# Optimization experiments

Hardware: AMD Instinct MI355X
Metric: run time of the kernel (lower is better)

The kernel has to match this reference:

```python
import jax, jax.numpy as jnp
import numpy as np

B, C, H, W = 16, 64, 256, 256
M1, M2 = 32, 32
SCALE = 1.0 / (C * C)


def setup_inputs() -> dict:
    key = jax.random.key(0)
    ks = jax.random.split(key, 5)
    x = jax.random.normal(ks[0], (B, C, H, W), dtype=jnp.float32)
    w1_real = SCALE * jax.random.uniform(ks[1], (C, C, M1, M2), dtype=jnp.float32)
    w1_imag = SCALE * jax.random.uniform(ks[2], (C, C, M1, M2), dtype=jnp.float32)
    w2_real = SCALE * jax.random.uniform(ks[3], (C, C, M1, M2), dtype=jnp.float32)
    w2_imag = SCALE * jax.random.uniform(ks[4], (C, C, M1, M2), dtype=jnp.float32)
    return {"x": x, "w1_real": w1_real, "w1_imag": w1_imag,
            "w2_real": w2_real, "w2_imag": w2_imag}


def reference(x, w1_real, w1_imag, w2_real, w2_imag):
    # x: (B, C, H, W) real. rfft2 over last two dims -> (B, C, H, W//2+1) complex64
    x_ft = jnp.fft.rfft2(x)
    # compl_mul2d in the source reduces to an elementwise multiply by the
    # weights summed over their FIRST (in_channels) axis:
    #   out[b,c,m1,m2] = x_ft[b,c,m1,m2] * sum_j weights[j,c,m1,m2]
    w1 = (w1_real + 1j * w1_imag).sum(axis=0)  # (C, M1, M2) complex
    w2 = (w2_real + 1j * w2_imag).sum(axis=0)  # (C, M1, M2) complex
    out_ft = jnp.zeros_like(x_ft)
    out_ft = out_ft.at[:, :, :M1, :M2].set(x_ft[:, :, :M1, :M2] * w1[None])
    out_ft = out_ft.at[:, :, -M1:, :M2].set(x_ft[:, :, -M1:, :M2] * w2[None])
    return jnp.fft.irfft2(out_ft, s=(H, W))
```

## Files before the change

kernel.cpp:

```cpp
#include <hip/hip_runtime.h>
#include <math.h>

#define TWO_PI 6.28318530717958647692f

typedef __attribute__((ext_vector_type(8))) short bf16x8;
typedef __attribute__((ext_vector_type(4))) float f32x4;
typedef __attribute__((ext_vector_type(4))) short short4v;

#define MFMA16(A,B,C) __builtin_amdgcn_mfma_f32_16x16x32_bf16((A),(B),(C),0,0,0)


#define C_B2H 0
#define C_B2L 16384
#define C_C1H 32768
#define C_C1L 49152
#define C_S1H 65536
#define C_S1L 81920
#define C_SNH 98304
#define C_SNL 114688
#define C_A1H 131072
#define C_A1L 163840
#define C_DH  196608
#define C_DL  212992

__device__ __forceinline__ unsigned short bhi(float v) {
    union { float f; unsigned u; } x; x.f = v;
    return (unsigned short)(x.u >> 16);
}
__device__ __forceinline__ float bval(unsigned short h) {
    union { unsigned u; float f; } x; x.u = ((unsigned)h) << 16;
    return x.f;
}
__device__ __forceinline__ void split2(float v, unsigned short& hi, unsigned short& lo) {
    hi = bhi(v);
    lo = bhi(v - bval(hi));
}

__global__ __launch_bounds__(256)
void const_kernel(unsigned short* __restrict__ cst) {
    int e = blockIdx.x * 256 + threadIdx.x;
    const float w0 = TWO_PI / 256.0f;
    float v; int i, baseH, baseL;
    if (e < 16384) {
        i = e; baseH = C_B2H; baseL = C_B2L;
        int j = i & 7, lane = (i >> 3) & 63, tt = i >> 9;
        int nt = tt & 3, kt = tt >> 2;
        int k = kt * 32 + (lane >> 4) * 8 + j;
        int n = nt * 16 + (lane & 15);
        int fr = n & 31;
        float s_, c_;
        sincosf(w0 * (float)((fr * k) & 255), &s_, &c_);
        v = (n < 32) ? c_ : -s_;
    } else if (e < 65536) {
        int mid = (e - 16384) >> 14;
        i = (e - 16384) & 16383;
        baseH = C_C1H + mid * 32768; baseL = baseH + 16384;
        int j = i & 7, lane = (i >> 3) & 63, tt = i >> 9;
        int mt = tt & 3, kt = tt >> 2;
        int s = mt * 16 + (lane & 15);
        int h = kt * 32 + (lane >> 4) * 8 + j;
        int f = (s < 32) ? s : s + 192;
        float s_, c_;
        sincosf(w0 * (float)((f * h) & 255), &s_, &c_);
        v = (mid == 0) ? c_ : ((mid == 1) ? s_ : -s_);
    } else if (e < 98304) {
        i = e - 65536; baseH = C_A1H; baseL = C_A1L;
        int j = i & 7, lane = (i >> 3) & 63, tt = i >> 9;
        int mt = tt & 15, kt = tt >> 4;
        int h = mt * 16 + (lane & 15);
        int k = kt * 32 + (lane >> 4) * 8 + j;
        int s = k & 63;
        int f = (s < 32) ? s : s + 192;
        float s_, c_;
        sincosf(w0 * (float)((f * h) & 255), &s_, &c_);
        v = (k < 64) ? c_ : s_;
    } else {
        i = e - 98304; baseH = C_DH; baseL = C_DL;
        int j = i & 7, lane = (i >> 3) & 63, tt = i >> 9;
        int nt = tt & 15, kt = tt >> 4;
        int wc = nt * 16 + (lane & 15);
        int k = kt * 32 + (lane >> 4) * 8 + j;
        int k2 = k & 31;
        float a = (k2 == 0) ? 1.f : 2.f;
        float s_, c_;
        sincosf(w0 * (float)((k2 * wc) & 255), &s_, &c_);
        v = (k < 32) ? a * c_ : -a * s_;
    }
    unsigned short hi, lo; split2(v, hi, lo);
    cst[baseH + i] = hi;
    cst[baseL + i] = lo;
}

__global__ __launch_bounds__(256)
void wsum_part(const float* __restrict__ w1r, const float* __restrict__ w1i,
               const float* __restrict__ w2r, const float* __restrict__ w2i,
               float4* __restrict__ part) {
    const int jp = blockIdx.x >> 6;
    const int e4 = (blockIdx.x & 63) * 256 + threadIdx.x;
    const float4* A = (const float4*)w1r;
    const float4* Bv = (const float4*)w1i;
    const float4* Cv = (const float4*)w2r;
    const float4* Dv = (const float4*)w2i;
    float4 a = make_float4(0.f,0.f,0.f,0.f), b = a, c = a, d = a;
    #pragma unroll
    for (int jj = 0; jj < 8; ++jj) {
        int idx = (jp * 8 + jj) * 16384 + e4;
        float4 v;
        v = A[idx];  a.x += v.x; a.y += v.y; a.z += v.z; a.w += v.w;
        v = Bv[idx]; b.x += v.x; b.y += v.y; b.z += v.z; b.w += v.w;
        v = Cv[idx]; c.x += v.x; c.y += v.y; c.z += v.z; c.w += v.w;
        v = Dv[idx]; d.x += v.x; d.y += v.y; d.z += v.z; d.w += v.w;
    }
    part[(0 * 8 + jp) * 16384 + e4] = a;
    part[(1 * 8 + jp) * 16384 + e4] = b;
    part[(2 * 8 + jp) * 16384 + e4] = c;
    part[(3 * 8 + jp) * 16384 + e4] = d;
}

__global__ __launch_bounds__(256)
void wsum_reduce(const float4* __restrict__ part,
                 float4* __restrict__ s1, float4* __restrict__ s2) {
    const int e4 = blockIdx.x * 256 + threadIdx.x;
    float4 a = make_float4(0.f,0.f,0.f,0.f), b = a, c = a, d = a;
    #pragma unroll
    for (int jp = 0; jp < 8; ++jp) {
        float4 v;
        v = part[(0 * 8 + jp) * 16384 + e4]; a.x += v.x; a.y += v.y; a.z += v.z; a.w += v.w;
        v = part[(1 * 8 + jp) * 16384 + e4]; b.x += v.x; b.y += v.y; b.z += v.z; b.w += v.w;
        v = part[(2 * 8 + jp) * 16384 + e4]; c.x += v.x; c.y += v.y; c.z += v.z; c.w += v.w;
        v = part[(3 * 8 + jp) * 16384 + e4]; d.x += v.x; d.y += v.y; d.z += v.z; d.w += v.w;
    }
    const float sc = 1.0f / 65536.0f;
    s1[e4 * 2]     = make_float4(a.x * sc, b.x * sc, a.y * sc, b.y * sc);
    s1[e4 * 2 + 1] = make_float4(a.z * sc, b.z * sc, a.w * sc, b.w * sc);
    s2[e4 * 2]     = make_float4(c.x * sc, d.x * sc, c.y * sc, d.y * sc);
    s2[e4 * 2 + 1] = make_float4(c.z * sc, d.z * sc, c.w * sc, d.w * sc);
}

__global__ __launch_bounds__(256)
void fwd_kernel(const float* __restrict__ x, float* __restrict__ X,
                const unsigned short* __restrict__ cst) {
    const int img = blockIdx.x;
    const int t = threadIdx.x;
    const int lane = t & 63;
    const int wv = t >> 6;

    __shared__ unsigned short xs_hi[8192], xs_lo[8192];
    __shared__ unsigned short yt_hi[2048], yt_lo[2048];

    f32x4 acc[4];
    #pragma unroll
    for (int i = 0; i < 4; ++i) { acc[i].x = 0; acc[i].y = 0; acc[i].z = 0; acc[i].w = 0; }

    const int mt2  = wv >> 1;
    const int nt2b = (wv & 1) * 2;

    const float* xim = x + (size_t)img * 65536;
    const int r_st  = t >> 3;
    const int c4_st = t & 7;
    const float4* src = (const float4*)xim + r_st * 64 + c4_st;

    float4 pre[8];
    #pragma unroll
    for (int i = 0; i < 8; ++i) pre[i] = src[i * 8];

    #pragma unroll 1
    for (int hc = 0; hc < 8; ++hc) {
        {
            #pragma unroll
            for (int i = 0; i < 8; ++i) {
                float4 vx = pre[i];
                int cc = (c4_st + i * 8) * 4;
                int idx = (r_st * 256 + cc) ^ ((r_st & 7) << 3);
                unsigned short h0,l0,h1,l1,h2,l2,h3,l3;
                split2(vx.x, h0, l0); split2(vx.y, h1, l1);
                split2(vx.z, h2, l2); split2(vx.w, h3, l3);
                short4v vh, vl;
                vh.x=(short)h0; vh.y=(short)h1; vh.z=(short)h2; vh.w=(short)h3;
                vl.x=(short)l0; vl.y=(short)l1; vl.z=(short)l2; vl.w=(short)l3;
                *(short4v*)&xs_hi[idx] = vh;
                *(short4v*)&xs_lo[idx] = vl;
            }
        }
        __syncthreads();
        if (hc < 7) {
            const float4* nsrc = src + (hc + 1) * 2048;
            #pragma unroll
            for (int i = 0; i < 8; ++i) pre[i] = nsrc[i * 8];
        }
        f32x4 acc2[2];
        acc2[0].x=0; acc2[0].y=0; acc2[0].z=0; acc2[0].w=0;
        acc2[1].x=0; acc2[1].y=0; acc2[1].z=0; acc2[1].w=0;
        {
            const int mrow = mt2 * 16 + (lane & 15);
            const int kb = (lane >> 4) * 8;
            #pragma unroll
            for (int kt = 0; kt < 8; ++kt) {
                int aidx = (mrow * 256 + kt * 32 + kb) ^ ((mrow & 7) << 3);
                bf16x8 ah = *(const bf16x8*)&xs_hi[aidx];
                bf16x8 al = *(const bf16x8*)&xs_lo[aidx];
                #pragma unroll
                for (int q = 0; q < 2; ++q) {
                    int boff = ((kt * 4 + nt2b + q) * 64 + lane) * 8;
                    bf16x8 bh = *(const bf16x8*)&cst[C_B2H + boff];
                    bf16x8 bl = *(const bf16x8*)&cst[C_B2L + boff];
                    acc2[q] = MFMA16(ah, bh, acc2[q]);
                    acc2[q] = MFMA16(ah, bl, acc2[q]);
                    acc2[q] = MFMA16(al, bh, acc2[q]);
                }
            }
        }
        {
            const int hbase = mt2 * 16 + (lane >> 4) * 4;
            #pragma unroll
            for (int q = 0; q < 2; ++q) {
                int n = (nt2b + q) * 16 + (lane & 15);
                int idx = (n * 32 + hbase) ^ ((n & 7) << 3);
                short4v vh, vl; unsigned short hh, ll;
                split2(acc2[q][0], hh, ll); vh.x=(short)hh; vl.x=(short)ll;
                split2(acc2[q][1], hh, ll); vh.y=(short)hh; vl.y=(short)ll;
                split2(acc2[q][2], hh, ll); vh.z=(short)hh; vl.z=(short)ll;
                split2(acc2[q][3], hh, ll); vh.w=(short)hh; vl.w=(short)ll;
                *(short4v*)&yt_hi[idx] = vh;
                *(short4v*)&yt_lo[idx] = vl;
            }
        }
        __syncthreads();
        {
            const int aoff = ((hc * 4 + wv) * 64 + lane) * 8;
            bf16x8 c1h = *(const bf16x8*)&cst[C_C1H + aoff];
            bf16x8 c1l = *(const bf16x8*)&cst[C_C1L + aoff];
            bf16x8 s1h = *(const bf16x8*)&cst[C_S1H + aoff];
            bf16x8 s1l = *(const bf16x8*)&cst[C_S1L + aoff];
            bf16x8 snh = *(const bf16x8*)&cst[C_SNH + aoff];
            bf16x8 snl = *(const bf16x8*)&cst[C_SNL + aoff];
            const int kl = (lane >> 4) * 8;
            #pragma unroll
            for (int nt = 0; nt < 4; ++nt) {
                int nRe = (nt & 1) * 16 + (lane & 15);
                int nIm = 32 + nRe;
                int reIdx = (nRe * 32 + kl) ^ ((nRe & 7) << 3);
                int imIdx = (nIm * 32 + kl) ^ ((nIm & 7) << 3);
                bf16x8 brh = *(const bf16x8*)&yt_hi[reIdx];
                bf16x8 brl = *(const bf16x8*)&yt_lo[reIdx];
                bf16x8 bih = *(const bf16x8*)&yt_hi[imIdx];
                bf16x8 bil = *(const bf16x8*)&yt_lo[imIdx];
                if (nt < 2) {
                    acc[nt] = MFMA16(c1h, brh, acc[nt]);
                    acc[nt] = MFMA16(c1h, brl, acc[nt]);
                    acc[nt] = MFMA16(c1l, brh, acc[nt]);
                    acc[nt] = MFMA16(s1h, bih, acc[nt]);
                    acc[nt] = MFMA16(s1h, bil, acc[nt]);
                    acc[nt] = MFMA16(s1l, bih, acc[nt]);
                } else {
                    acc[nt] = MFMA16(c1h, bih, acc[nt]);
                    acc[nt] = MFMA16(c1h, bil, acc[nt]);
                    acc[nt] = MFMA16(c1l, bih, acc[nt]);
                    acc[nt] = MFMA16(snh, brh, acc[nt]);
                    acc[nt] = MFMA16(snh, brl, acc[nt]);
                    acc[nt] = MFMA16(snl, brh, acc[nt]);
                }
            }
        }
        __syncthreads();
    }
    {
        float* Xp = X + (size_t)img * 4096;
        const int sbase = wv * 16 + (lane >> 4) * 4;
        #pragma unroll
        for (int nt = 0; nt < 4; ++nt) {
            int n = nt * 16 + (lane & 15);
            #pragma unroll
            for (int r = 0; r < 4; ++r)
                Xp[(sbase + r) * 64 + n] = acc[nt][r];
        }
    }
}

__global__ __launch_bounds__(256)
void inv_kernel(const float* __restrict__ X, const float2* __restrict__ s1,
                const float2* __restrict__ s2, float* __restrict__ out,
                const unsigned short* __restrict__ cst) {
    const int img = blockIdx.x;
    const int c = img & 63;
    const int t = threadIdx.x;
    const int lane = t & 63;
    const int wv = t >> 6;

    __shared__ unsigned short lds[32768];
    unsigned short* GTh = lds;
    unsigned short* GTl = lds + 8192;
    unsigned short* Th  = lds;
    unsigned short* Tl  = lds + 16384;

    {
        const float* Xp = X + (size_t)img * 4096;
        int s = t >> 2;
        int k2b = (t & 3) * 8;
        const float2* wp = (s < 32) ? (s1 + c * 1024 + s * 32 + k2b)
                                    : (s2 + c * 1024 + (s - 32) * 32 + k2b);
        float4 xr0 = *(const float4*)&Xp[s * 64 + k2b];
        float4 xr1 = *(const float4*)&Xp[s * 64 + k2b + 4];
        float4 xi0 = *(const float4*)&Xp[s * 64 + 32 + k2b];
        float4 xi1 = *(const float4*)&Xp[s * 64 + 32 + k2b + 4];
        float xr[8] = {xr0.x,xr0.y,xr0.z,xr0.w,xr1.x,xr1.y,xr1.z,xr1.w};
        float xi[8] = {xi0.x,xi0.y,xi0.z,xi0.w,xi1.x,xi1.y,xi1.z,xi1.w};
        #pragma unroll
        for (int i = 0; i < 8; ++i) {
            int k2 = k2b + i;
            float2 wvv = wp[i];
            float gr = xr[i]*wvv.x - xi[i]*wvv.y;
            float gi = xr[i]*wvv.y + xi[i]*wvv.x;
            unsigned short grh, grl, gih, gil;
            split2(gr, grh, grl); split2(gi, gih, gil);
            int swz = (k2 & 7) << 3;
            int i0 = (k2 * 128 + s) ^ swz;
            int i1 = ((32 + k2) * 128 + s) ^ swz;
            int i2 = (k2 * 128 + 64 + s) ^ swz;
            int i3 = ((32 + k2) * 128 + 64 + s) ^ swz;
            GTh[i0] = grh; GTl[i0] = grl;
            GTh[i1] = gih; GTl[i1] = gil;
            GTh[i2] = (unsigned short)(gih ^ 0x8000u);
            GTl[i2] = (unsigned short)(gil ^ 0x8000u);
            GTh[i3] = grh; GTl[i3] = grl;
        }
    }
    __syncthreads();

    f32x4 Tacc[4][4];
    #pragma unroll
    for (int a = 0; a < 4; ++a)
        #pragma unroll
        for (int b = 0; b < 4; ++b) { Tacc[a][b].x=0; Tacc[a][b].y=0; Tacc[a][b].z=0; Tacc[a][b].w=0; }
    {
        const int kb = (lane >> 4) * 8;
        #pragma unroll
        for (int kt = 0; kt < 4; ++kt) {
            bf16x8 bh[4], bl[4];
            #pragma unroll
            for (int nt = 0; nt < 4; ++nt) {
                int n = nt * 16 + (lane & 15);
                int idx = (n * 128 + kt * 32 + kb) ^ ((n & 7) << 3);
                bh[nt] = *(const bf16x8*)&GTh[idx];
                bl[nt] = *(const bf16x8*)&GTl[idx];
            }
            #pragma unroll
            for (int mi = 0; mi < 4; ++mi) {
                int aoff = ((kt * 16 + 4 * wv + mi) * 64 + lane) * 8;
                bf16x8 ah = *(const bf16x8*)&cst[C_A1H + aoff];
                bf16x8 al = *(const bf16x8*)&cst[C_A1L + aoff];
                #pragma unroll
                for (int nt = 0; nt < 4; ++nt) {
                    Tacc[mi][nt] = MFMA16(ah, bh[nt], Tacc[mi][nt]);
                    Tacc[mi][nt] = MFMA16(ah, bl[nt], Tacc[mi][nt]);
                    Tacc[mi][nt] = MFMA16(al, bh[nt], Tacc[mi][nt]);
                }
            }
        }
    }
    __syncthreads();

    {
        #pragma unroll
        for (int mi = 0; mi < 4; ++mi) {
            int m0 = (4 * wv + mi) * 16 + (lane >> 4) * 4;
            #pragma unroll
            for (int nt = 0; nt < 4; ++nt) {
                int k = nt * 16 + (lane & 15);
                #pragma unroll
                for (int r = 0; r < 4; ++r) {
                    int m = m0 + r;
                    int idx = (m * 64 + k) ^ ((m & 7) << 3);
                    unsigned short hh, ll; split2(Tacc[mi][nt][r], hh, ll);
                    Th[idx] = hh; Tl[idx] = ll;
                }
            }
        }
    }
    __syncthreads();

    float* oim = out + (size_t)img * 65536;
    const int kb2 = (lane >> 4) * 8;
    #pragma unroll 1
    for (int strip = 0; strip < 4; ++strip) {
        f32x4 oacc[4][4];
        #pragma unroll
        for (int a = 0; a < 4; ++a)
            #pragma unroll
            for (int b = 0; b < 4; ++b) { oacc[a][b].x=0; oacc[a][b].y=0; oacc[a][b].z=0; oacc[a][b].w=0; }
        #pragma unroll
        for (int kt = 0; kt < 2; ++kt) {
            bf16x8 ah[4], al[4];
            #pragma unroll
            for (int mi = 0; mi < 4; ++mi) {
                int m = (strip * 4 + mi) * 16 + (lane & 15);
                int idx = (m * 64 + kt * 32 + kb2) ^ ((m & 7) << 3);
                ah[mi] = *(const bf16x8*)&Th[idx];
                al[mi] = *(const bf16x8*)&Tl[idx];
            }
            #pragma unroll
            for (int ni = 0; ni < 4; ++ni) {
                int boff = ((kt * 16 + 4 * wv + ni) * 64 + lane) * 8;
                bf16x8 bh = *(const bf16x8*)&cst[C_DH + boff];
                bf16x8 bl = *(const bf16x8*)&cst[C_DL + boff];
                #pragma unroll
                for (int mi = 0; mi < 4; ++mi) {
                    oacc[mi][ni] = MFMA16(ah[mi], bh, oacc[mi][ni]);
                    oacc[mi][ni] = MFMA16(ah[mi], bl, oacc[mi][ni]);
                    oacc[mi][ni] = MFMA16(al[mi], bh, oacc[mi][ni]);
                }
            }
        }
        #pragma unroll
        for (int mi = 0; mi < 4; ++mi) {
            int h = strip * 64 + mi * 16 + (lane >> 4) * 4;
            #pragma unroll
            for (int ni = 0; ni < 4; ++ni) {
                int wc = (4 * wv + ni) * 16 + (lane & 15);
                #pragma unroll
                for (int r = 0; r < 4; ++r)
                    oim[(size_t)(h + r) * 256 + wc] = oacc[mi][ni][r];
            }
        }
    }
}

extern "C" void kernel_launch(void* const* d_in, const int* in_sizes, int n_in,
                              void* d_out, int out_size, void* d_ws, size_t ws_size,
                              hipStream_t stream) {
    const float* x   = (const float*)d_in[0];
    const float* w1r = (const float*)d_in[1];
    const float* w1i = (const float*)d_in[2];
    const float* w2r = (const float*)d_in[3];
    const float* w2i = (const float*)d_in[4];
    float* out = (float*)d_out;

    char* ws = (char*)d_ws;
    float* X   = (float*)ws;
    float2* s1 = (float2*)(ws + 16777216);
    float2* s2 = (float2*)(ws + 16777216 + 524288);
    unsigned short* cst = (unsigned short*)(ws + 17825792);
    float4* part = (float4*)ws;

    hipLaunchKernelGGL(const_kernel, dim3(448), dim3(256), 0, stream, cst);
    hipLaunchKernelGGL(wsum_part, dim3(512), dim3(256), 0, stream,
                       w1r, w1i, w2r, w2i, part);
    hipLaunchKernelGGL(wsum_reduce, dim3(64), dim3(256), 0, stream,
                       part, (float4*)s1, (float4*)s2);
    hipLaunchKernelGGL(fwd_kernel, dim3(1024), dim3(256), 0, stream, x, X, cst);
    hipLaunchKernelGGL(inv_kernel, dim3(1024), dim3(256), 0, stream, X, s1, s2, out, cst);
}
```

Before: 552.5 us.

## Fuse forward and inverse spectral kernels, keeping spectrum in registers

Merges fwd_kernel and inv_kernel into one kernel per image. The truncated spectrum stays in MFMA accumulators, is multiplied by the summed weights preloaded into registers, and is written straight into LDS as split bf16 hi/lo operands. This removes the global round trip of the intermediate X buffer and one kernel launch. In exchange the fused kernel uses more LDS (a 64KB shared buffer plus yt arrays) and more registers, which may lower occupancy.

```diff
diff --git a/kernel.cpp b/kernel.cpp
--- a/kernel.cpp
+++ b/kernel.cpp
@@ -138,15 +138,30 @@
 }
 
 __global__ __launch_bounds__(256)
-void fwd_kernel(const float* __restrict__ x, float* __restrict__ X,
-                const unsigned short* __restrict__ cst) {
+void fused_kernel(const float* __restrict__ x,
+                  const float2* __restrict__ s1, const float2* __restrict__ s2,
+                  float* __restrict__ out, const unsigned short* __restrict__ cst) {
     const int img = blockIdx.x;
+    const int c = img & 63;
     const int t = threadIdx.x;
     const int lane = t & 63;
     const int wv = t >> 6;
 
-    __shared__ unsigned short xs_hi[8192], xs_lo[8192];
+    __shared__ unsigned short lds[32768];
     __shared__ unsigned short yt_hi[2048], yt_lo[2048];
+    unsigned short* xs_hi = lds;
+    unsigned short* xs_lo = lds + 8192;
+
+    float2 wreg[2][4];
+    {
+        const float2* wbase = ((wv < 2) ? s1 : s2) + c * 1024
+                              + ((wv & 1) * 16 + (lane >> 4) * 4) * 32;
+        #pragma unroll
+        for (int r = 0; r < 4; ++r) {
+            wreg[0][r] = wbase[r * 32 + (lane & 15)];
+            wreg[1][r] = wbase[r * 32 + 16 + (lane & 15)];
+        }
+    }
 
     f32x4 acc[4];
     #pragma unroll
@@ -264,69 +279,43 @@
         }
         __syncthreads();
     }
+
     {
-        float* Xp = X + (size_t)img * 4096;
-        const int sbase = wv * 16 + (lane >> 4) * 4;
-        #pragma unroll
-        for (int nt = 0; nt < 4; ++nt) {
-            int n = nt * 16 + (lane & 15);
-            #pragma unroll
-            for (int r = 0; r < 4; ++r)
-                Xp[(sbase + r) * 64 + n] = acc[nt][r];
-        }
-    }
-}
-
-__global__ __launch_bounds__(256)
-void inv_kernel(const float* __restrict__ X, const float2* __restrict__ s1,
-                const float2* __restrict__ s2, float* __restrict__ out,
-                const unsigned short* __restrict__ cst) {
-    const int img = blockIdx.x;
-    const int c = img & 63;
-    const int t = threadIdx.x;
-    const int lane = t & 63;
-    const int wv = t >> 6;
-
-    __shared__ unsigned short lds[32768];
+        unsigned short* GTh = lds;
+        unsigned short* GTl = lds + 8192;
+        const int l15 = lane & 15;
+        const int s0 = wv * 16 + (lane >> 4) * 4;
+        #pragma unroll
+        for (int j = 0; j < 2; ++j) {
+            int k2 = j * 16 + l15;
+            int col = s0 ^ ((k2 & 7) << 3);
+            short4v grh, grl, gih, gil, ngh, ngl;
+            #pragma unroll
+            for (int r = 0; r < 4; ++r) {
+                float xr = acc[j][r], xi = acc[2 + j][r];
+                float wr = wreg[j][r].x, wi = wreg[j][r].y;
+                float gr = xr * wr - xi * wi;
+                float gi = xr * wi + xi * wr;
+                unsigned short h1, l1, h2, l2;
+                split2(gr, h1, l1); split2(gi, h2, l2);
+                grh[r] = (short)h1; grl[r] = (short)l1;
+                gih[r] = (short)h2; gil[r] = (short)l2;
+                ngh[r] = (short)(h2 ^ 0x8000u); ngl[r] = (short)(l2 ^ 0x8000u);
+            }
+            *(short4v*)&GTh[k2 * 128 + col] = grh;
+            *(short4v*)&GTl[k2 * 128 + col] = grl;
+            *(short4v*)&GTh[(32 + k2) * 128 + col] = gih;
+            *(short4v*)&GTl[(32 + k2) * 128 + col] = gil;
+            *(short4v*)&GTh[k2 * 128 + 64 + col] = ngh;
+            *(short4v*)&GTl[k2 * 128 + 64 + col] = ngl;
+            *(short4v*)&GTh[(32 + k2) * 128 + 64 + col] = grh;
+            *(short4v*)&GTl[(32 + k2) * 128 + 64 + col] = grl;
+        }
+    }
+    __syncthreads();
+
     unsigned short* GTh = lds;
     unsigned short* GTl = lds + 8192;
-    unsigned short* Th  = lds;
-    unsigned short* Tl  = lds + 16384;
-
-    {
-        const float* Xp = X + (size_t)img * 4096;
-        int s = t >> 2;
-        int k2b = (t & 3) * 8;
-        const float2* wp = (s < 32) ? (s1 + c * 1024 + s * 32 + k2b)
-                                    : (s2 + c * 1024 + (s - 32) * 32 + k2b);
-        float4 xr0 = *(const float4*)&Xp[s * 64 + k2b];
-        float4 xr1 = *(const float4*)&Xp[s * 64 + k2b + 4];
-        float4 xi0 = *(const float4*)&Xp[s * 64 + 32 + k2b];
-        float4 xi1 = *(const float4*)&Xp[s * 64 + 32 + k2b + 4];
-        float xr[8] = {xr0.x,xr0.y,xr0.z,xr0.w,xr1.x,xr1.y,xr1.z,xr1.w};
-        float xi[8] = {xi0.x,xi0.y,xi0.z,xi0.w,xi1.x,xi1.y,xi1.z,xi1.w};
-        #pragma unroll
-        for (int i = 0; i < 8; ++i) {
-            int k2 = k2b + i;
-            float2 wvv = wp[i];
-            float gr = xr[i]*wvv.x - xi[i]*wvv.y;
-            float gi = xr[i]*wvv.y + xi[i]*wvv.x;
-            unsigned short grh, grl, gih, gil;
-            split2(gr, grh, grl); split2(gi, gih, gil);
-            int swz = (k2 & 7) << 3;
-            int i0 = (k2 * 128 + s) ^ swz;
-            int i1 = ((32 + k2) * 128 + s) ^ swz;
-            int i2 = (k2 * 128 + 64 + s) ^ swz;
-            int i3 = ((32 + k2) * 128 + 64 + s) ^ swz;
-            GTh[i0] = grh; GTl[i0] = grl;
-            GTh[i1] = gih; GTl[i1] = gil;
-            GTh[i2] = (unsigned short)(gih ^ 0x8000u);
-            GTl[i2] = (unsigned short)(gil ^ 0x8000u);
-            GTh[i3] = grh; GTl[i3] = grl;
-        }
-    }
-    __syncthreads();
-
     f32x4 Tacc[4][4];
     #pragma unroll
     for (int a = 0; a < 4; ++a)
@@ -360,6 +349,8 @@
     }
     __syncthreads();
 
+    unsigned short* Th = lds;
+    unsigned short* Tl = lds + 16384;
     {
         #pragma unroll
         for (int mi = 0; mi < 4; ++mi) {
@@ -436,17 +427,16 @@
     float* out = (float*)d_out;
 
     char* ws = (char*)d_ws;
-    float* X   = (float*)ws;
+    float4* part = (float4*)ws;
     float2* s1 = (float2*)(ws + 16777216);
     float2* s2 = (float2*)(ws + 16777216 + 524288);
     unsigned short* cst = (unsigned short*)(ws + 17825792);
-    float4* part = (float4*)ws;
 
     hipLaunchKernelGGL(const_kernel, dim3(448), dim3(256), 0, stream, cst);
     hipLaunchKernelGGL(wsum_part, dim3(512), dim3(256), 0, stream,
                        w1r, w1i, w2r, w2i, part);
     hipLaunchKernelGGL(wsum_reduce, dim3(64), dim3(256), 0, stream,
                        part, (float4*)s1, (float4*)s2);
-    hipLaunchKernelGGL(fwd_kernel, dim3(1024), dim3(256), 0, stream, x, X, cst);
-    hipLaunchKernelGGL(inv_kernel, dim3(1024), dim3(256), 0, stream, X, s1, s2, out, cst);
-}
+    hipLaunchKernelGGL(fused_kernel, dim3(1024), dim3(256), 0, stream,
+                       x, s1, s2, out, cst);
+}
```

Result: no change. 544.7 us (-1.4%).
